# Kernel tuning notes

Measured on AMD Instinct MI355X. Metric: run time of the kernel, lower is better.

Reference implementation:

```python
import jax, jax.numpy as jnp
import numpy as np

N_NODES = 100000
N_EDGES = 1600000
F_IN, HID, N_CLS = 128, 64, 40


def gcn_conv(x, src, dst, W, b, n_nodes):
    # x: [N, Fin] -> [N, Fout]; edges already include self-loops.
    h = x @ W  # [N, Fout]
    ones = jnp.ones_like(src, dtype=h.dtype)
    deg = jax.ops.segment_sum(ones, dst, num_segments=n_nodes)  # [N]
    dinv = jnp.where(deg > 0, jax.lax.rsqrt(deg), 0.0)
    norm = dinv[src] * dinv[dst]  # [E]
    msg = h[src] * norm[:, None]  # gather + scale
    out = jax.ops.segment_sum(msg, dst, num_segments=n_nodes)  # scatter-sum
    return out + b


def setup_inputs() -> dict:
    key = jax.random.key(0)
    ks = jax.random.split(key, 8)
    x = jax.random.normal(ks[0], (N_NODES, F_IN), dtype=jnp.float32)
    edge_index = jax.random.randint(ks[1], (2, N_EDGES), 0, N_NODES, dtype=jnp.int64)

    def glorot(k, fi, fo):
        s = float(np.sqrt(6.0 / (fi + fo)))
        return jax.random.uniform(k, (fi, fo), jnp.float32, -s, s)

    return {
        "x": x,
        "edge_index": edge_index,
        "W1": glorot(ks[2], F_IN, HID), "b1": jnp.zeros((HID,), jnp.float32),
        "W2": glorot(ks[3], HID, HID), "b2": jnp.zeros((HID,), jnp.float32),
        "W3": glorot(ks[4], HID, N_CLS), "b3": jnp.zeros((N_CLS,), jnp.float32),
    }


def reference(x, edge_index, W1, b1, W2, b2, W3, b3):
    n = x.shape[0]
    loop = jnp.arange(n, dtype=edge_index.dtype)
    src = jnp.concatenate([edge_index[0], loop])  # add self-loops
    dst = jnp.concatenate([edge_index[1], loop])
    # layer 1..3: GCNConv -> relu -> dropout(eval: identity)
    h = jax.nn.relu(gcn_conv(x, src, dst, W1, b1, n))
    h = jax.nn.relu(gcn_conv(h, src, dst, W2, b2, n))
    h = jax.nn.relu(gcn_conv(h, src, dst, W3, b3, n))
    return jax.nn.log_softmax(h, axis=1)
```

## Files before the change

kernel.cpp:

```cpp
#include <hip/hip_runtime.h>
#include <math.h>

typedef _Float16 half8   __attribute__((ext_vector_type(8)));
typedef float    float4v __attribute__((ext_vector_type(4)));

#define CAP 6144

static __device__ __forceinline__ unsigned short f32_to_f16u(float f) {
    _Float16 h = (_Float16)f;
    return __builtin_bit_cast(unsigned short, h);
}


__global__ __launch_bounds__(256) void prep_init(
    const float* __restrict__ W1, const float* __restrict__ W2, const float* __restrict__ W3,
    unsigned short* __restrict__ Wf1, unsigned short* __restrict__ Wf2,
    unsigned short* __restrict__ Wf3, int* __restrict__ bcur, int NB)
{
    if (blockIdx.x == 3) {
        for (int i = threadIdx.x; i < NB; i += 256) bcur[i] = 0;
        return;
    }
    const float* W; unsigned short* Wf; int K, M;
    if (blockIdx.x == 0)      { W = W1; Wf = Wf1; K = 128; M = 64; }
    else if (blockIdx.x == 1) { W = W2; Wf = Wf2; K = 64;  M = 64; }
    else                      { W = W3; Wf = Wf3; K = 64;  M = 40; }
    const int NT = (M + 15) >> 4, NTC = NT << 4, KS = K >> 5;
    for (int i = threadIdx.x; i < K * NTC; i += 256) {
        int k = i / NTC, nn = i - k * NTC;
        unsigned short hv = 0;
        if (nn < M) hv = f32_to_f16u(W[(size_t)k * M + nn]);
        int s = k >> 5, q = (k >> 3) & 3, j = k & 7;
        int u = nn >> 4, lane = (q << 4) | (nn & 15);
        Wf[((u * KS + s) << 9) + (lane << 3) + j] = hv;
    }
}


__global__ __launch_bounds__(256) void bin_edges(
    const int* __restrict__ src, const int* __restrict__ dst,
    int* __restrict__ bcur, unsigned int* __restrict__ bint, int E, int NB)
{
    __shared__ int h[512];
    __shared__ int rbase[512];
    const int tid = threadIdx.x;
    h[tid] = 0; h[tid + 256] = 0;
    __syncthreads();
    const int eb = blockIdx.x * 4096 + tid;
    int d[16], sr[16];
    #pragma unroll
    for (int k = 0; k < 16; ++k) {
        int i = eb + k * 256;
        if (i < E) {
            d[k] = dst[i]; sr[k] = src[i];
            atomicAdd(&h[d[k] >> 8], 1);
        } else d[k] = -1;
    }
    __syncthreads();
    for (int j = tid; j < NB; j += 256) {
        int c = h[j];
        rbase[j] = c ? atomicAdd(&bcur[j], c) : 0;
        h[j] = 0;
    }
    __syncthreads();
    #pragma unroll
    for (int k = 0; k < 16; ++k) {
        if (d[k] >= 0) {
            int bkt = d[k] >> 8;
            int pos = rbase[bkt] + atomicAdd(&h[bkt], 1);
            if (pos < CAP)
                bint[(size_t)bkt * CAP + pos] =
                    ((unsigned int)sr[k] << 8) | (unsigned int)(d[k] & 255);
        }
    }
}


__global__ __launch_bounds__(256) void build_csr(
    const unsigned int* __restrict__ bint, const int* __restrict__ bcur,
    int2* __restrict__ rp2, float* __restrict__ dinv, int* __restrict__ es, int n)
{
    __shared__ int cnt[256];
    __shared__ int sc[256];
    __shared__ int cur[256];
    const int b = blockIdx.x, tid = threadIdx.x;
    int total = bcur[b]; if (total > CAP) total = CAP;
    const unsigned int* bp = bint + (size_t)b * CAP;
    int* ep = es + (size_t)b * CAP;
    const int base = b * CAP;

    cnt[tid] = 0;
    __syncthreads();
    for (int i = tid; i < total; i += 256)
        atomicAdd(&cnt[bp[i] & 255], 1);
    __syncthreads();

    int v = cnt[tid];
    sc[tid] = v;
    __syncthreads();
    for (int off = 1; off < 256; off <<= 1) {
        int x = (tid >= off) ? sc[tid - off] : 0;
        __syncthreads();
        sc[tid] += x;
        __syncthreads();
    }
    int excl = sc[tid] - v;
    int node = (b << 8) + tid;
    if (node < n) {
        rp2[node]  = make_int2(base + excl, base + excl + v);
        dinv[node] = rsqrtf((float)(v + 1));
    }
    cur[tid] = excl;
    __syncthreads();

    for (int i = tid; i < total; i += 256) {
        unsigned int p = bp[i];
        int pos = atomicAdd(&cur[p & 255], 1);
        ep[pos] = (int)(p >> 8);
    }
}


template<int KK, int NT, int STRIDE, int MOUT, bool INF32>
__global__ __launch_bounds__(256) void gemm_t(
    const void* __restrict__ Xin, const unsigned short* __restrict__ Wf,
    const float* __restrict__ dinv, unsigned short* __restrict__ H, int n)
{
    constexpr int KS = KK >> 5;
    __shared__ __align__(16) unsigned short ldsA[4 * KS * 512];
    const int tid = threadIdx.x;
    const int n0  = blockIdx.x * 64;

    half8 bf[NT * KS];
    {
        const int lane = tid & 63;
        #pragma unroll
        for (int u = 0; u < NT; ++u)
            #pragma unroll
            for (int s = 0; s < KS; ++s)
                bf[u * KS + s] = *(const half8*)&Wf[((u * KS + s) << 9) + (lane << 3)];
    }

    {
        const int rl = tid >> 3;
        const int kl = tid & 7;
        #pragma unroll
        for (int rb = 0; rb < 64; rb += 32) {
            int r = rl + rb;
            int node = n0 + r;
            int t = r >> 4, m = r & 15;
            #pragma unroll
            for (int kq8 = 0; kq8 < (KK >> 2); kq8 += 8) {
                int k0 = (kl + kq8) << 2;
                unsigned short h[4] = {0, 0, 0, 0};
                if (node < n) {
                    if (INF32) {
                        const float* xp = (const float*)Xin + (size_t)node * KK + k0;
                        float4v v = *(const float4v*)xp;
                        #pragma unroll
                        for (int i = 0; i < 4; ++i) h[i] = f32_to_f16u(v[i]);
                    } else {
                        const unsigned int* ap =
                            (const unsigned int*)Xin + (((size_t)node * KK + k0) >> 1);
                        uint2 v = *(const uint2*)ap;
                        h[0] = (unsigned short)(v.x & 0xffff);
                        h[1] = (unsigned short)(v.x >> 16);
                        h[2] = (unsigned short)(v.y & 0xffff);
                        h[3] = (unsigned short)(v.y >> 16);
                    }
                }
                int s = k0 >> 5, q = (k0 >> 3) & 3, j0 = k0 & 7;
                int lane = (q << 4) | m;
                unsigned short* p = &ldsA[((t * KS + s) << 9) + (lane << 3) + j0];
                unsigned int lo = (unsigned int)h[0] | ((unsigned int)h[1] << 16);
                unsigned int hi = (unsigned int)h[2] | ((unsigned int)h[3] << 16);
                *(uint2*)p = make_uint2(lo, hi);
            }
        }
    }

    __syncthreads();

    const int wv   = tid >> 6;
    const int lane = tid & 63;
    float4v acc[NT];
    #pragma unroll
    for (int u = 0; u < NT; ++u) acc[u] = (float4v){0.f, 0.f, 0.f, 0.f};

    #pragma unroll
    for (int s = 0; s < KS; ++s) {
        half8 a = *(const half8*)&ldsA[((wv * KS + s) << 9) + (lane << 3)];
        #pragma unroll
        for (int u = 0; u < NT; ++u)
            acc[u] = __builtin_amdgcn_mfma_f32_16x16x32_f16(a, bf[u * KS + s], acc[u], 0, 0, 0);
    }

    const int mcol = lane & 15;
    const int quad = lane >> 4;
    #pragma unroll
    for (int reg = 0; reg < 4; ++reg) {
        int node = n0 + (wv << 4) + (quad << 2) + reg;
        if (node >= n) continue;
        float dv = dinv[node];
        #pragma unroll
        for (int u = 0; u < NT; ++u) {
            int col = (u << 4) + mcol;
            if (col < MOUT)
                H[(size_t)node * STRIDE + col] = f32_to_f16u(acc[u][reg] * dv);
        }
    }
}


template<int MOUT, int ROWU4>
__global__ __launch_bounds__(256) void gather_t(
    const int2* __restrict__ rp2, const int* __restrict__ es,
    const unsigned short* __restrict__ H, const float* __restrict__ dinv,
    const float* __restrict__ bias, unsigned short* __restrict__ Aout, int n)
{
    const int lane   = threadIdx.x & 63;
    const int half   = lane >> 5;
    const int lane32 = lane & 31;
    const int slot   = (lane >> 3) & 3;
    const int c8     = lane & 7;
    const bool act   = c8 < ROWU4;
    const uint4* H4  = (const uint4*)H;

    float bi[8];
    #pragma unroll
    for (int i = 0; i < 8; ++i) bi[i] = bias[(c8 << 3) + i];

    const half8 hz = {(_Float16)0, (_Float16)0, (_Float16)0, (_Float16)0,
                      (_Float16)0, (_Float16)0, (_Float16)0, (_Float16)0};

    const int TW2 = (int)(gridDim.x << 3);
    for (int nb = (((int)blockIdx.x << 2) + ((int)threadIdx.x >> 6)) << 1; nb < n; nb += TW2) {
        const int node = nb + half;
        const int2 e = rp2[node];
        const float dv = dinv[node];

        half8 hacc = hz;
        if (slot == 0 && act)
            hacc = __builtin_bit_cast(half8, H4[(size_t)node * ROWU4 + c8]);

        for (int cb = e.x; cb < e.y; cb += 32) {
            const int rem = e.y - cb;
            int eidx = cb + lane32; if (eidx > e.y - 1) eidx = e.y - 1;
            const int ei = es[eidx];
            #pragma unroll
            for (int j = 0; j < 8; ++j) {
                const int idx = (j << 2) + slot;
                const int s = __shfl(ei, (half << 5) + idx, 64);
                if (idx < rem && act)
                    hacc = hacc + __builtin_bit_cast(half8, H4[(size_t)s * ROWU4 + c8]);
            }
        }

        #pragma unroll
        for (int step = 8; step <= 16; step <<= 1) {
            uint4 u = __builtin_bit_cast(uint4, hacc);
            uint4 o;
            o.x = __shfl_xor(u.x, step, 64);
            o.y = __shfl_xor(u.y, step, 64);
            o.z = __shfl_xor(u.z, step, 64);
            o.w = __shfl_xor(u.w, step, 64);
            hacc = hacc + __builtin_bit_cast(half8, o);
        }

        if (slot == 0) {
            unsigned short o[8];
            #pragma unroll
            for (int i = 0; i < 8; ++i)
                o[i] = f32_to_f16u(fmaxf((float)hacc[i] * dv + bi[i], 0.0f));
            uint4 w;
            w.x = (unsigned int)o[0] | ((unsigned int)o[1] << 16);
            w.y = (unsigned int)o[2] | ((unsigned int)o[3] << 16);
            w.z = (unsigned int)o[4] | ((unsigned int)o[5] << 16);
            w.w = (unsigned int)o[6] | ((unsigned int)o[7] << 16);
            ((uint4*)Aout)[(size_t)node * 8 + c8] = w;
        }
    }
}


template<int MOUT, int ROWU4>
__global__ __launch_bounds__(256) void gather_softmax(
    const int2* __restrict__ rp2, const int* __restrict__ es,
    const unsigned short* __restrict__ H, const float* __restrict__ dinv,
    const float* __restrict__ bias, float* __restrict__ out, int n)
{
    const int lane   = threadIdx.x & 63;
    const int half   = lane >> 5;
    const int lane32 = lane & 31;
    const int slot   = (lane >> 3) & 3;
    const int c8     = lane & 7;
    const bool act   = c8 < ROWU4;
    const uint4* H4  = (const uint4*)H;

    float bi[8];
    #pragma unroll
    for (int i = 0; i < 8; ++i) {
        int col = (c8 << 3) + i;
        bi[i] = (col < MOUT) ? bias[col] : 0.0f;
    }

    const half8 hz = {(_Float16)0, (_Float16)0, (_Float16)0, (_Float16)0,
                      (_Float16)0, (_Float16)0, (_Float16)0, (_Float16)0};

    const int TW2 = (int)(gridDim.x << 3);
    for (int nb = (((int)blockIdx.x << 2) + ((int)threadIdx.x >> 6)) << 1; nb < n; nb += TW2) {
        const int node = nb + half;
        const int2 e = rp2[node];
        const float dv = dinv[node];

        half8 hacc = hz;
        if (slot == 0 && act)
            hacc = __builtin_bit_cast(half8, H4[(size_t)node * ROWU4 + c8]);

        for (int cb = e.x; cb < e.y; cb += 32) {
            const int rem = e.y - cb;
            int eidx = cb + lane32; if (eidx > e.y - 1) eidx = e.y - 1;
            const int ei = es[eidx];
            #pragma unroll
            for (int j = 0; j < 8; ++j) {
                const int idx = (j << 2) + slot;
                const int s = __shfl(ei, (half << 5) + idx, 64);
                if (idx < rem && act)
                    hacc = hacc + __builtin_bit_cast(half8, H4[(size_t)s * ROWU4 + c8]);
            }
        }

        #pragma unroll
        for (int step = 8; step <= 16; step <<= 1) {
            uint4 u = __builtin_bit_cast(uint4, hacc);
            uint4 o;
            o.x = __shfl_xor(u.x, step, 64);
            o.y = __shfl_xor(u.y, step, 64);
            o.z = __shfl_xor(u.z, step, 64);
            o.w = __shfl_xor(u.w, step, 64);
            hacc = hacc + __builtin_bit_cast(half8, o);
        }

        float z[8]; float m = -INFINITY;
        #pragma unroll
        for (int i = 0; i < 8; ++i) {
            int col = (c8 << 3) + i;
            z[i] = (col < MOUT && act) ? fmaxf((float)hacc[i] * dv + bi[i], 0.0f)
                                       : -INFINITY;
            m = fmaxf(m, z[i]);
        }
        m = fmaxf(m, __shfl_xor(m, 1, 64));
        m = fmaxf(m, __shfl_xor(m, 2, 64));
        m = fmaxf(m, __shfl_xor(m, 4, 64));
        float s = 0.0f;
        #pragma unroll
        for (int i = 0; i < 8; ++i) s += expf(z[i] - m);
        s += __shfl_xor(s, 1, 64);
        s += __shfl_xor(s, 2, 64);
        s += __shfl_xor(s, 4, 64);
        float ls = logf(s) + m;
        if (slot == 0 && c8 < (MOUT + 7) / 8) {
            float* op = out + (size_t)node * MOUT + (c8 << 3);
            float4v o0 = {z[0] - ls, z[1] - ls, z[2] - ls, z[3] - ls};
            float4v o1 = {z[4] - ls, z[5] - ls, z[6] - ls, z[7] - ls};
            *(float4v*)op = o0;
            *(float4v*)(op + 4) = o1;
        }
    }
}


extern "C" void kernel_launch(void* const* d_in, const int* in_sizes, int n_in,
                              void* d_out, int out_size, void* d_ws, size_t ws_size,
                              hipStream_t stream)
{
    const float* x  = (const float*)d_in[0];
    const int*   ei = (const int*)  d_in[1];
    const float* W1 = (const float*)d_in[2];
    const float* b1 = (const float*)d_in[3];
    const float* W2 = (const float*)d_in[4];
    const float* b2 = (const float*)d_in[5];
    const float* W3 = (const float*)d_in[6];
    const float* b3 = (const float*)d_in[7];

    const int F_IN = 128;
    const int n = in_sizes[0] / F_IN;
    const int E = in_sizes[1] / 2;
    const int* src = ei;
    const int* dst = ei + E;
    float* out = (float*)d_out;

    const int NB = (n + 255) >> 8;

    auto align = [](size_t v) { return (v + 255) & ~(size_t)255; };
    char* w = (char*)d_ws;
    size_t off = 0;
    float*          dinv = (float*)(w + off);          off = align(off + (size_t)n * 4);
    unsigned short* H1   = (unsigned short*)(w + off); off = align(off + (size_t)n * 64 * 2);
    unsigned short* A    = (unsigned short*)(w + off); off = align(off + (size_t)n * 64 * 2);
    unsigned short* H3   = (unsigned short*)(w + off); off = align(off + (size_t)n * 40 * 2);
    int2*           rp2  = (int2*)(w + off);           off = align(off + (size_t)n * 8);
    int*            es   = (int*)(w + off);            off = align(off + (size_t)NB * CAP * 4);
    unsigned int*   bint = (unsigned int*)(w + off);   off = align(off + (size_t)NB * CAP * 4);
    int*            bcur = (int*)(w + off);            off = align(off + (size_t)512 * 4);
    unsigned short* Wf1  = (unsigned short*)(w + off); off = align(off + (size_t)8192 * 2);
    unsigned short* Wf2  = (unsigned short*)(w + off); off = align(off + (size_t)4096 * 2);
    unsigned short* Wf3  = (unsigned short*)(w + off); off = align(off + (size_t)3072 * 2);
    unsigned short* H2   = H1;

    const int BLK = 256;
    auto cdiv = [](int a, int b) { return (a + b - 1) / b; };
    const int EB = cdiv(E, 4096);
    const int GB = cdiv(n, 64);
    const int GG = 2048;

    prep_init<<<4, BLK, 0, stream>>>(W1, W2, W3, Wf1, Wf2, Wf3, bcur, NB);
    bin_edges<<<EB, BLK, 0, stream>>>(src, dst, bcur, bint, E, NB);
    build_csr<<<NB, BLK, 0, stream>>>(bint, bcur, rp2, dinv, es, n);

    gemm_t<128, 4, 64, 64, true><<<GB, BLK, 0, stream>>>(x, Wf1, dinv, H1, n);
    gather_t<64, 8><<<GG, BLK, 0, stream>>>(rp2, es, H1, dinv, b1, A, n);

    gemm_t<64, 4, 64, 64, false><<<GB, BLK, 0, stream>>>(A, Wf2, dinv, H2, n);
    gather_t<64, 8><<<GG, BLK, 0, stream>>>(rp2, es, H2, dinv, b2, A, n);

    gemm_t<64, 3, 40, 40, false><<<GB, BLK, 0, stream>>>(A, Wf3, dinv, H3, n);
    gather_softmax<40, 5><<<GG, BLK, 0, stream>>>(rp2, es, H3, dinv, b3, out, n);
}
```

Baseline: 276.2 us.

## Load GEMM A-tiles directly to registers and remap softmax gather lanes

The GEMM kernel drops its LDS staging and barrier. Each lane now loads its own MFMA A-fragment straight from global memory, converting from f32 in the first layer, and out-of-range rows are clamped to the last node. The final gather+log-softmax kernel moves from two nodes per wave with 8-lane groups to one node per wave with 12 groups of 5 lanes, which fits the 40-column rows. A shuffle tree sums the 12 partial results. This aims to raise lane use and memory parallelism in the last layer and cut LDS traffic in the GEMMs, but the GEMM loads may coalesce less well than the staged version.

```diff
diff --git a/kernel.cpp b/kernel.cpp
--- a/kernel.cpp
+++ b/kernel.cpp
@@ -127,86 +127,59 @@
     const float* __restrict__ dinv, unsigned short* __restrict__ H, int n)
 {
     constexpr int KS = KK >> 5;
-    __shared__ __align__(16) unsigned short ldsA[4 * KS * 512];
-    const int tid = threadIdx.x;
-    const int n0  = blockIdx.x * 64;
-
-    half8 bf[NT * KS];
-    {
-        const int lane = tid & 63;
-        #pragma unroll
-        for (int u = 0; u < NT; ++u)
-            #pragma unroll
-            for (int s = 0; s < KS; ++s)
-                bf[u * KS + s] = *(const half8*)&Wf[((u * KS + s) << 9) + (lane << 3)];
-    }
-
-    {
-        const int rl = tid >> 3;
-        const int kl = tid & 7;
-        #pragma unroll
-        for (int rb = 0; rb < 64; rb += 32) {
-            int r = rl + rb;
-            int node = n0 + r;
-            int t = r >> 4, m = r & 15;
-            #pragma unroll
-            for (int kq8 = 0; kq8 < (KK >> 2); kq8 += 8) {
-                int k0 = (kl + kq8) << 2;
-                unsigned short h[4] = {0, 0, 0, 0};
-                if (node < n) {
-                    if (INF32) {
-                        const float* xp = (const float*)Xin + (size_t)node * KK + k0;
-                        float4v v = *(const float4v*)xp;
-                        #pragma unroll
-                        for (int i = 0; i < 4; ++i) h[i] = f32_to_f16u(v[i]);
-                    } else {
-                        const unsigned int* ap =
-                            (const unsigned int*)Xin + (((size_t)node * KK + k0) >> 1);
-                        uint2 v = *(const uint2*)ap;
-                        h[0] = (unsigned short)(v.x & 0xffff);
-                        h[1] = (unsigned short)(v.x >> 16);
-                        h[2] = (unsigned short)(v.y & 0xffff);
-                        h[3] = (unsigned short)(v.y >> 16);
-                    }
-                }
-                int s = k0 >> 5, q = (k0 >> 3) & 3, j0 = k0 & 7;
-                int lane = (q << 4) | m;
-                unsigned short* p = &ldsA[((t * KS + s) << 9) + (lane << 3) + j0];
-                unsigned int lo = (unsigned int)h[0] | ((unsigned int)h[1] << 16);
-                unsigned int hi = (unsigned int)h[2] | ((unsigned int)h[3] << 16);
-                *(uint2*)p = make_uint2(lo, hi);
-            }
-        }
-    }
-
-    __syncthreads();
-
+    const int tid  = threadIdx.x;
     const int wv   = tid >> 6;
     const int lane = tid & 63;
+    const int quad = lane >> 4;
+    const int mrow = lane & 15;
+    const int n0   = blockIdx.x * 64 + (wv << 4);
+
+    half8 bf[NT * KS];
+    #pragma unroll
+    for (int u = 0; u < NT; ++u)
+        #pragma unroll
+        for (int s = 0; s < KS; ++s)
+            bf[u * KS + s] = *(const half8*)&Wf[((u * KS + s) << 9) + (lane << 3)];
+
+    int node  = n0 + mrow;
+    int nodeL = node < n ? node : (n - 1);
+
     float4v acc[NT];
     #pragma unroll
     for (int u = 0; u < NT; ++u) acc[u] = (float4v){0.f, 0.f, 0.f, 0.f};
 
     #pragma unroll
     for (int s = 0; s < KS; ++s) {
-        half8 a = *(const half8*)&ldsA[((wv * KS + s) << 9) + (lane << 3)];
+        const int k0 = (s << 5) + (quad << 3);
+        half8 a;
+        if (INF32) {
+            const float* xp = (const float*)Xin + (size_t)nodeL * KK + k0;
+            float4v v0 = *(const float4v*)xp;
+            float4v v1 = *(const float4v*)(xp + 4);
+            #pragma unroll
+            for (int i = 0; i < 4; ++i) {
+                a[i]     = (_Float16)v0[i];
+                a[4 + i] = (_Float16)v1[i];
+            }
+        } else {
+            a = *(const half8*)((const unsigned short*)Xin + (size_t)nodeL * 64 + k0);
+        }
         #pragma unroll
         for (int u = 0; u < NT; ++u)
             acc[u] = __builtin_amdgcn_mfma_f32_16x16x32_f16(a, bf[u * KS + s], acc[u], 0, 0, 0);
     }
 
     const int mcol = lane & 15;
-    const int quad = lane >> 4;
     #pragma unroll
     for (int reg = 0; reg < 4; ++reg) {
-        int node = n0 + (wv << 4) + (quad << 2) + reg;
-        if (node >= n) continue;
-        float dv = dinv[node];
+        int onode = n0 + (quad << 2) + reg;
+        if (onode >= n) continue;
+        float dv = dinv[onode];
         #pragma unroll
         for (int u = 0; u < NT; ++u) {
             int col = (u << 4) + mcol;
             if (col < MOUT)
-                H[(size_t)node * STRIDE + col] = f32_to_f16u(acc[u][reg] * dv);
+                H[(size_t)onode * STRIDE + col] = f32_to_f16u(acc[u][reg] * dv);
         }
     }
 }
@@ -283,70 +256,69 @@
 }
 
 
-template<int MOUT, int ROWU4>
+template<int MOUT>
 __global__ __launch_bounds__(256) void gather_softmax(
     const int2* __restrict__ rp2, const int* __restrict__ es,
     const unsigned short* __restrict__ H, const float* __restrict__ dinv,
     const float* __restrict__ bias, float* __restrict__ out, int n)
 {
-    const int lane   = threadIdx.x & 63;
-    const int half   = lane >> 5;
-    const int lane32 = lane & 31;
-    const int slot   = (lane >> 3) & 3;
-    const int c8     = lane & 7;
-    const bool act   = c8 < ROWU4;
-    const uint4* H4  = (const uint4*)H;
+    const int lane = threadIdx.x & 63;
+    const int slot = lane / 5;
+    const int c5   = lane - slot * 5;
+    const bool act = slot < 12;
+    const uint4* H4 = (const uint4*)H;
 
     float bi[8];
     #pragma unroll
     for (int i = 0; i < 8; ++i) {
-        int col = (c8 << 3) + i;
+        int col = (c5 << 3) + i;
         bi[i] = (col < MOUT) ? bias[col] : 0.0f;
     }
 
     const half8 hz = {(_Float16)0, (_Float16)0, (_Float16)0, (_Float16)0,
                       (_Float16)0, (_Float16)0, (_Float16)0, (_Float16)0};
 
-    const int TW2 = (int)(gridDim.x << 3);
-    for (int nb = (((int)blockIdx.x << 2) + ((int)threadIdx.x >> 6)) << 1; nb < n; nb += TW2) {
-        const int node = nb + half;
+    const int NW = (int)(gridDim.x << 2);
+    for (int node = ((int)blockIdx.x << 2) + ((int)threadIdx.x >> 6); node < n; node += NW) {
         const int2 e = rp2[node];
         const float dv = dinv[node];
 
         half8 hacc = hz;
-        if (slot == 0 && act)
-            hacc = __builtin_bit_cast(half8, H4[(size_t)node * ROWU4 + c8]);
-
-        for (int cb = e.x; cb < e.y; cb += 32) {
-            const int rem = e.y - cb;
-            int eidx = cb + lane32; if (eidx > e.y - 1) eidx = e.y - 1;
+        if (slot == 0)
+            hacc = __builtin_bit_cast(half8, H4[(size_t)node * 5 + c5]);
+
+        for (int cb = e.x; cb < e.y; cb += 64) {
+            int rem = e.y - cb; if (rem > 64) rem = 64;
+            int eidx = cb + lane; if (eidx > e.y - 1) eidx = e.y - 1;
             const int ei = es[eidx];
             #pragma unroll
-            for (int j = 0; j < 8; ++j) {
-                const int idx = (j << 2) + slot;
-                const int s = __shfl(ei, (half << 5) + idx, 64);
+            for (int j = 0; j < 6; ++j) {
+                const int idx = j * 12 + slot;
+                const int s = __shfl(ei, idx & 63, 64);
                 if (idx < rem && act)
-                    hacc = hacc + __builtin_bit_cast(half8, H4[(size_t)s * ROWU4 + c8]);
+                    hacc = hacc + __builtin_bit_cast(half8, H4[(size_t)s * 5 + c5]);
             }
         }
 
         #pragma unroll
-        for (int step = 8; step <= 16; step <<= 1) {
+        for (int step = 8; step >= 1; step >>= 1) {
+            const int srcl = (lane + 5 * step) & 63;
             uint4 u = __builtin_bit_cast(uint4, hacc);
             uint4 o;
-            o.x = __shfl_xor(u.x, step, 64);
-            o.y = __shfl_xor(u.y, step, 64);
-            o.z = __shfl_xor(u.z, step, 64);
-            o.w = __shfl_xor(u.w, step, 64);
-            hacc = hacc + __builtin_bit_cast(half8, o);
+            o.x = __shfl(u.x, srcl, 64);
+            o.y = __shfl(u.y, srcl, 64);
+            o.z = __shfl(u.z, srcl, 64);
+            o.w = __shfl(u.w, srcl, 64);
+            if (slot < step && slot + step < 12)
+                hacc = hacc + __builtin_bit_cast(half8, o);
         }
 
         float z[8]; float m = -INFINITY;
         #pragma unroll
         for (int i = 0; i < 8; ++i) {
-            int col = (c8 << 3) + i;
-            z[i] = (col < MOUT && act) ? fmaxf((float)hacc[i] * dv + bi[i], 0.0f)
-                                       : -INFINITY;
+            int col = (c5 << 3) + i;
+            z[i] = (slot == 0 && col < MOUT)
+                       ? fmaxf((float)hacc[i] * dv + bi[i], 0.0f) : -INFINITY;
             m = fmaxf(m, z[i]);
         }
         m = fmaxf(m, __shfl_xor(m, 1, 64));
@@ -359,8 +331,8 @@
         s += __shfl_xor(s, 2, 64);
         s += __shfl_xor(s, 4, 64);
         float ls = logf(s) + m;
-        if (slot == 0 && c8 < (MOUT + 7) / 8) {
-            float* op = out + (size_t)node * MOUT + (c8 << 3);
+        if (slot == 0) {
+            float* op = out + (size_t)node * MOUT + (c5 << 3);
             float4v o0 = {z[0] - ls, z[1] - ls, z[2] - ls, z[3] - ls};
             float4v o1 = {z[4] - ls, z[5] - ls, z[6] - ls, z[7] - ls};
             *(float4v*)op = o0;
@@ -425,5 +397,5 @@
     gather_t<64, 8><<<GG, BLK, 0, stream>>>(rp2, es, H2, dinv, b2, A, n);
 
     gemm_t<64, 3, 40, 40, false><<<GB, BLK, 0, stream>>>(A, Wf3, dinv, H3, n);
-    gather_softmax<40, 5><<<GG, BLK, 0, stream>>>(rp2, es, H3, dinv, b3, out, n);
-}
+    gather_softmax<40><<<GG, BLK, 0, stream>>>(rp2, es, H3, dinv, b3, out, n);
+}
```

After: 296.2 us. 1.07x slower.
